# Optimization experiments

Measured on AMD Instinct MI355X. Metric: run time of the kernel, lower is better.

Reference implementation:

```python
import jax, jax.numpy as jnp
import numpy as np

B, S, H, L, V = 128, 512, 1024, 4, 32000


def setup_inputs() -> dict:
    key = jax.random.key(0)
    ks = jax.random.split(key, 7)
    lengths = jax.random.randint(ks[0], (B,), 1, S + 1)
    lengths = lengths.at[0].set(S)  # force max length == S so T is static
    tok = jax.random.randint(ks[1], (B, S), 1, V)  # nonzero tokens inside length
    pos = jnp.arange(S)[None, :]
    x = jnp.where(pos < lengths[:, None], tok, 0)  # 0 = pad (x>0 defines length)
    emb = jax.random.normal(ks[2], (V, H), dtype=jnp.float32) * 0.02
    W_ih = jax.random.normal(ks[3], (L, 4 * H, H), dtype=jnp.float32) / np.float32(np.sqrt(H))
    W_hh = jax.random.normal(ks[4], (L, 4 * H, H), dtype=jnp.float32) / np.float32(np.sqrt(H))
    b_ih = jax.random.normal(ks[5], (L, 4 * H), dtype=jnp.float32) * 0.01
    b_hh = jax.random.normal(ks[6], (L, 4 * H), dtype=jnp.float32) * 0.01
    return {"x": x, "emb": emb, "W_ih": W_ih, "W_hh": W_hh, "b_ih": b_ih, "b_hh": b_hh}


def reference(x, emb, W_ih, W_hh, b_ih, b_hh):
    # lengths and pack's descending sort (pack_padded_sequence, enforce_sorted=False)
    lengths = jnp.sum(x > 0, axis=1)                         # [B]
    sorted_idx = jnp.argsort(-lengths, stable=True)          # sorted (desc) order
    unsort_idx = jnp.argsort(sorted_idx)                     # packed.unsorted_indices

    # Source bug: `start` is never advanced, so every iteration runs a ONE-step
    # stacked LSTM (zero init state) on packed.data[0:bs_t] == t=0 embeddings of
    # the bs_t longest sequences. Compute that single step once on all rows.
    xt = emb[x[sorted_idx, 0]]                               # [B, H] sorted order
    h0 = jnp.zeros_like(xt)                                  # zero initial hidden
    hs, cs = [], []
    for l in range(W_ih.shape[0]):
        gates = xt @ W_ih[l].T + b_ih[l] + h0 @ W_hh[l].T + b_hh[l]
        i, f, g, o = jnp.split(gates, 4, axis=-1)            # torch LSTMCell order
        c = jax.nn.sigmoid(i) * jnp.tanh(g)                  # f * c0 = 0
        h = jax.nn.sigmoid(o) * jnp.tanh(c)
        xt = h
        hs.append(h)
        cs.append(c)

    # output[t, b] = top-layer h for original seq b, zeroed where t >= lengths[b]
    T = x.shape[1]                                           # max length == S
    h_top = xt[unsort_idx]                                   # back to original order
    tmask = (jnp.arange(T)[:, None] < lengths[None, :]).astype(h_top.dtype)  # [T,B]
    output = tmask[:, :, None] * h_top[None, :, :]           # [T, B, H]

    # state from the LAST loop iteration: sorted order, rows >= bs_last zero-padded
    bs_last = jnp.sum(lengths >= T)                          # batch size at t = T-1
    smask = (jnp.arange(x.shape[0]) < bs_last).astype(h_top.dtype)[None, :, None]
    state_h = jnp.stack(hs, axis=0) * smask                  # [L, B, H]
    state_c = jnp.stack(cs, axis=0) * smask                  # [L, B, H]
    return output, state_h, state_c
```

## Files before the change

### kernel.cpp

```cpp
#include <hip/hip_runtime.h>

#define Bn 128
#define Sn 512
#define Hn 1024
#define Ln 4

typedef float nfloat4 __attribute__((ext_vector_type(4)));
typedef __attribute__((ext_vector_type(8))) short short8;
typedef __attribute__((ext_vector_type(4))) float f32x4;

__device__ __forceinline__ float sigmoidf_(float x) { return 1.0f / (1.0f + __expf(-x)); }

__device__ __forceinline__ unsigned short bf16hi(float f) {
  unsigned u = __float_as_uint(f);
  u = u + 0x7FFFu + ((u >> 16) & 1u);
  return (unsigned short)(u >> 16);
}
__device__ __forceinline__ float bf16tof(unsigned short h) {
  return __uint_as_float(((unsigned)h) << 16);
}

__global__ __launch_bounds__(128) void len_kernel(const int* __restrict__ x, int* __restrict__ lengths) {
  const int b = blockIdx.x, t = threadIdx.x;
  int4 v = ((const int4*)x)[b * 128 + t];
  int c = (v.x > 0) + (v.y > 0) + (v.z > 0) + (v.w > 0);
  for (int off = 32; off > 0; off >>= 1) c += __shfl_down(c, off);
  __shared__ int tmp[2];
  if ((t & 63) == 0) tmp[t >> 6] = c;
  __syncthreads();
  if (t == 0) lengths[b] = tmp[0] + tmp[1];
}

__global__ __launch_bounds__(128) void sort_kernel(const int* __restrict__ x, const int* __restrict__ lengths,
                                                   int* __restrict__ rank, int* __restrict__ tok_sorted,
                                                   int* __restrict__ bs_last) {
  __shared__ int sl[128];
  __shared__ int cnt;
  const int b = threadIdx.x;
  const int len = lengths[b];
  sl[b] = len;
  if (b == 0) cnt = 0;
  __syncthreads();
  int r = 0;
  for (int b2 = 0; b2 < 128; b2++) {
    int l2 = sl[b2];
    r += (l2 > len) || (l2 == len && b2 < b);
  }
  rank[b] = r;
  tok_sorted[r] = x[b * Sn];
  if (len >= Sn) atomicAdd(&cnt, 1);
  __syncthreads();
  if (b == 0) bs_last[0] = cnt;
}

__global__ __launch_bounds__(256) void gather_cvt(const int* __restrict__ tok_sorted,
                                                  const float* __restrict__ emb,
                                                  unsigned short* __restrict__ xhi,
                                                  unsigned short* __restrict__ xlo) {
  const int r = blockIdx.x, t = threadIdx.x;
  const int tok = tok_sorted[r];
  float4 v = ((const float4*)emb)[(size_t)tok * 256 + t];
  float f[4] = {v.x, v.y, v.z, v.w};
  unsigned short hh[4], ll[4];
#pragma unroll
  for (int j = 0; j < 4; j++) {
    hh[j] = bf16hi(f[j]);
    ll[j] = bf16hi(f[j] - bf16tof(hh[j]));
  }
  ((ushort4*)xhi)[r * 256 + t] = make_ushort4(hh[0], hh[1], hh[2], hh[3]);
  ((ushort4*)xlo)[r * 256 + t] = make_ushort4(ll[0], ll[1], ll[2], ll[3]);
}

__global__ __launch_bounds__(256) void gemm_mfma(const unsigned short* __restrict__ xhi,
                                                 const unsigned short* __restrict__ xlo,
                                                 const float* __restrict__ Wl,
                                                 float* __restrict__ part) {
  __shared__ unsigned short Whi[64][264];
  __shared__ unsigned short Wlo[64][264];
  const int t = threadIdx.x;
  const int bid = blockIdx.x;
  const int nt = bid % 48;
  const int kc = bid / 48;
  const int q = nt >> 4;
  const int qoff = (q == 0) ? 0 : ((q == 1) ? 2048 : 3072);
  const int mrow0 = qoff + (nt & 15) * 64;
  const int k0 = kc * 256;

#pragma unroll
  for (int i = 0; i < 16; i++) {
    const int vi = i * 256 + t;
    const int c = vi >> 6;
    const int ks4 = (vi & 63) * 4;
    float4 w4 = *(const float4*)&Wl[(size_t)(mrow0 + c) * 1024 + k0 + ks4];
    float f[4] = {w4.x, w4.y, w4.z, w4.w};
    unsigned short hh[4], ll[4];
#pragma unroll
    for (int j = 0; j < 4; j++) {
      hh[j] = bf16hi(f[j]);
      ll[j] = bf16hi(f[j] - bf16tof(hh[j]));
    }
    *(ushort4*)&Whi[c][ks4] = make_ushort4(hh[0], hh[1], hh[2], hh[3]);
    *(ushort4*)&Wlo[c][ks4] = make_ushort4(ll[0], ll[1], ll[2], ll[3]);
  }
  __syncthreads();

  const int w = t >> 6;
  const int l = t & 63;
  const int lrow = l & 15;
  const int lk8 = (l >> 4) * 8;

  f32x4 acc[2][4];
#pragma unroll
  for (int rt = 0; rt < 2; rt++)
#pragma unroll
    for (int ct = 0; ct < 4; ct++) acc[rt][ct] = (f32x4)0.0f;

  const unsigned short* xh0 = xhi + (size_t)(w * 32 + lrow) * 1024 + k0 + lk8;
  const unsigned short* xl0 = xlo + (size_t)(w * 32 + lrow) * 1024 + k0 + lk8;

#pragma unroll
  for (int ks = 0; ks < 8; ks++) {
    const int kk = ks * 32;
    short8 ah[2], al[2], bh[4], bl[4];
#pragma unroll
    for (int rt = 0; rt < 2; rt++) {
      ah[rt] = *(const short8*)(xh0 + rt * 16 * 1024 + kk);
      al[rt] = *(const short8*)(xl0 + rt * 16 * 1024 + kk);
    }
#pragma unroll
    for (int ct = 0; ct < 4; ct++) {
      bh[ct] = *(const short8*)&Whi[ct * 16 + lrow][kk + lk8];
      bl[ct] = *(const short8*)&Wlo[ct * 16 + lrow][kk + lk8];
    }
#pragma unroll
    for (int rt = 0; rt < 2; rt++)
#pragma unroll
      for (int ct = 0; ct < 4; ct++) {
        acc[rt][ct] = __builtin_amdgcn_mfma_f32_16x16x32_bf16(ah[rt], bh[ct], acc[rt][ct], 0, 0, 0);
        acc[rt][ct] = __builtin_amdgcn_mfma_f32_16x16x32_bf16(ah[rt], bl[ct], acc[rt][ct], 0, 0, 0);
        acc[rt][ct] = __builtin_amdgcn_mfma_f32_16x16x32_bf16(al[rt], bh[ct], acc[rt][ct], 0, 0, 0);
      }
  }

  const int rbase = w * 32 + (l >> 4) * 4;
#pragma unroll
  for (int rt = 0; rt < 2; rt++)
#pragma unroll
    for (int ct = 0; ct < 4; ct++) {
      const int m = (nt & 15) * 64 + ct * 16 + lrow;
      *(f32x4*)&part[(((size_t)kc * 3 + q) * 1024 + m) * 128 + rbase + rt * 16] = acc[rt][ct];
    }
}

__global__ __launch_bounds__(256) void act_kernel(const float* __restrict__ part,
                                                  const float* __restrict__ bih,
                                                  const float* __restrict__ bhh,
                                                  const int* __restrict__ bs_last,
                                                  float* __restrict__ xt_out,
                                                  float* __restrict__ sh,
                                                  float* __restrict__ sc,
                                                  unsigned short* __restrict__ xhi_out,
                                                  unsigned short* __restrict__ xlo_out) {
  __shared__ float red[128][12];
  const int t = threadIdx.x;
  const int r = t & 127;
  const int half = t >> 7;
  const int m0 = blockIdx.x * 4;
  float s[3][4];
#pragma unroll
  for (int qq = 0; qq < 3; qq++)
#pragma unroll
    for (int mm = 0; mm < 4; mm++) s[qq][mm] = 0.0f;
#pragma unroll
  for (int k2 = 0; k2 < 2; k2++) {
    const int kcc = half * 2 + k2;
#pragma unroll
    for (int qq = 0; qq < 3; qq++)
#pragma unroll
      for (int mm = 0; mm < 4; mm++)
        s[qq][mm] += part[(((size_t)kcc * 3 + qq) * 1024 + (m0 + mm)) * 128 + r];
  }
  if (half == 1) {
#pragma unroll
    for (int qq = 0; qq < 3; qq++)
#pragma unroll
      for (int mm = 0; mm < 4; mm++) red[r][qq * 4 + mm] = s[qq][mm];
  }
  __syncthreads();
  if (half == 0) {
    const int bs = bs_last[0];
    float hv[4], cv[4];
    unsigned short hh[4], ll[4];
#pragma unroll
    for (int mm = 0; mm < 4; mm++) {
      const int m = m0 + mm;
      const float si = s[0][mm] + red[r][0 * 4 + mm] + bih[m] + bhh[m];
      const float sg = s[1][mm] + red[r][1 * 4 + mm] + bih[2048 + m] + bhh[2048 + m];
      const float so = s[2][mm] + red[r][2 * 4 + mm] + bih[3072 + m] + bhh[3072 + m];
      const float c = sigmoidf_(si) * tanhf(sg);
      const float h = sigmoidf_(so) * tanhf(c);
      hv[mm] = h;
      cv[mm] = c;
      hh[mm] = bf16hi(h);
      ll[mm] = bf16hi(h - bf16tof(hh[mm]));
    }
    const float msk = (r < bs) ? 1.0f : 0.0f;
    *(float4*)&xt_out[(size_t)r * 1024 + m0] = make_float4(hv[0], hv[1], hv[2], hv[3]);
    *(float4*)&sh[(size_t)r * 1024 + m0] =
        make_float4(msk * hv[0], msk * hv[1], msk * hv[2], msk * hv[3]);
    *(float4*)&sc[(size_t)r * 1024 + m0] =
        make_float4(msk * cv[0], msk * cv[1], msk * cv[2], msk * cv[3]);
    *(ushort4*)&xhi_out[(size_t)r * 1024 + m0] = make_ushort4(hh[0], hh[1], hh[2], hh[3]);
    *(ushort4*)&xlo_out[(size_t)r * 1024 + m0] = make_ushort4(ll[0], ll[1], ll[2], ll[3]);
  }
}

__global__ __launch_bounds__(256) void bcast_kernel(const float* __restrict__ hfin,
                                                    const int* __restrict__ lengths,
                                                    const int* __restrict__ rank,
                                                    float* __restrict__ out) {
  const int b = blockIdx.x & 127;
  const int c = blockIdx.x >> 7;
  const int len = lengths[b];
  const int t0 = c * 64;
  nfloat4 v = (nfloat4)0.0f;
  if (t0 < len) v = ((const nfloat4*)hfin)[rank[b] * 256 + threadIdx.x];
  int valid = len - t0;
  valid = valid < 0 ? 0 : (valid > 64 ? 64 : valid);
  nfloat4* p = (nfloat4*)out + ((size_t)t0 * 128 + b) * 256 + threadIdx.x;
  for (int i = 0; i < valid; i++) {
    __builtin_nontemporal_store(v, p);
    p += 32768;
  }
  const nfloat4 z = (nfloat4)0.0f;
  for (int i = valid; i < 64; i++) {
    __builtin_nontemporal_store(z, p);
    p += 32768;
  }
}

extern "C" void kernel_launch(void* const* d_in, const int* in_sizes, int n_in,
                              void* d_out, int out_size, void* d_ws, size_t ws_size,
                              hipStream_t stream) {
  const int* x = (const int*)d_in[0];
  const float* emb = (const float*)d_in[1];
  const float* W_ih = (const float*)d_in[2];
  const float* b_ih = (const float*)d_in[4];
  const float* b_hh = (const float*)d_in[5];

  float* out = (float*)d_out;
  float* sh = out + (size_t)Sn * Bn * Hn;
  float* sc = sh + (size_t)Ln * Bn * Hn;
  float* part = out;
  unsigned short* bfbase = (unsigned short*)(out + (size_t)2097152);
  unsigned short* xhiA = bfbase;
  unsigned short* xloA = bfbase + 131072;
  unsigned short* xhiB = bfbase + 262144;
  unsigned short* xloB = bfbase + 393216;

  char* ws = (char*)d_ws;
  int* lengths = (int*)ws;
  int* rank = lengths + 128;
  int* tok_sorted = rank + 128;
  int* bs_last = tok_sorted + 128;
  float* xtA = (float*)(ws + 4096);
  float* xtB = xtA + 128 * 1024;

  len_kernel<<<128, 128, 0, stream>>>(x, lengths);
  sort_kernel<<<1, 128, 0, stream>>>(x, lengths, rank, tok_sorted, bs_last);
  gather_cvt<<<128, 256, 0, stream>>>(tok_sorted, emb, xhiA, xloA);

  float* xtF[2] = {xtA, xtB};
  unsigned short* hiP[2] = {xhiA, xhiB};
  unsigned short* loP[2] = {xloA, xloB};
  int cur = 0;
  for (int l = 0; l < Ln; l++) {
    const int nxt = cur ^ 1;
    gemm_mfma<<<192, 256, 0, stream>>>(hiP[cur], loP[cur], W_ih + (size_t)l * 4 * Hn * Hn, part);
    act_kernel<<<256, 256, 0, stream>>>(part, b_ih + l * 4 * Hn, b_hh + l * 4 * Hn, bs_last,
                                        xtF[l & 1], sh + (size_t)l * Bn * Hn,
                                        sc + (size_t)l * Bn * Hn, hiP[nxt], loP[nxt]);
    cur = nxt;
  }
  bcast_kernel<<<1024, 256, 0, stream>>>(xtF[1], lengths, rank, out);
}
```

Baseline: 475.9 us.

## Fuse LSTM gate GEMM with activation and overlap padding zero-stores in idle blocks

```diff
diff --git a/kernel.cpp b/kernel.cpp
--- a/kernel.cpp
+++ b/kernel.cpp
@@ -20,37 +20,46 @@
   return __uint_as_float(((unsigned)h) << 16);
 }
 
-__global__ __launch_bounds__(128) void len_kernel(const int* __restrict__ x, int* __restrict__ lengths) {
-  const int b = blockIdx.x, t = threadIdx.x;
-  int4 v = ((const int4*)x)[b * 128 + t];
-  int c = (v.x > 0) + (v.y > 0) + (v.z > 0) + (v.w > 0);
-  for (int off = 32; off > 0; off >>= 1) c += __shfl_down(c, off);
-  __shared__ int tmp[2];
-  if ((t & 63) == 0) tmp[t >> 6] = c;
-  __syncthreads();
-  if (t == 0) lengths[b] = tmp[0] + tmp[1];
-}
-
-__global__ __launch_bounds__(128) void sort_kernel(const int* __restrict__ x, const int* __restrict__ lengths,
-                                                   int* __restrict__ rank, int* __restrict__ tok_sorted,
-                                                   int* __restrict__ bs_last) {
+__global__ __launch_bounds__(1024) void lensort_kernel(const int* __restrict__ x,
+                                                       int* __restrict__ lengths,
+                                                       int* __restrict__ rank,
+                                                       int* __restrict__ tok_sorted,
+                                                       int* __restrict__ bs_last) {
+  __shared__ int pc[128][8];
   __shared__ int sl[128];
   __shared__ int cnt;
-  const int b = threadIdx.x;
-  const int len = lengths[b];
-  sl[b] = len;
-  if (b == 0) cnt = 0;
+  const int t = threadIdx.x;
+  const int row = t >> 3, seg = t & 7;
+  int c = 0;
+  const int4* xp = (const int4*)x + row * 128 + seg * 16;
+#pragma unroll
+  for (int i = 0; i < 16; i++) {
+    int4 v = xp[i];
+    c += (v.x > 0) + (v.y > 0) + (v.z > 0) + (v.w > 0);
+  }
+  pc[row][seg] = c;
+  if (t == 0) cnt = 0;
   __syncthreads();
-  int r = 0;
-  for (int b2 = 0; b2 < 128; b2++) {
-    int l2 = sl[b2];
-    r += (l2 > len) || (l2 == len && b2 < b);
-  }
-  rank[b] = r;
-  tok_sorted[r] = x[b * Sn];
-  if (len >= Sn) atomicAdd(&cnt, 1);
+  int len = 0;
+  if (t < 128) {
+#pragma unroll
+    for (int i = 0; i < 8; i++) len += pc[t][i];
+    sl[t] = len;
+    lengths[t] = len;
+  }
   __syncthreads();
-  if (b == 0) bs_last[0] = cnt;
+  if (t < 128) {
+    int r = 0;
+    for (int b2 = 0; b2 < 128; b2++) {
+      int l2 = sl[b2];
+      r += (l2 > len) || (l2 == len && b2 < t);
+    }
+    rank[t] = r;
+    tok_sorted[r] = x[t * Sn];
+    if (len >= Sn) atomicAdd(&cnt, 1);
+  }
+  __syncthreads();
+  if (t == 0) bs_last[0] = cnt;
 }
 
 __global__ __launch_bounds__(256) void gather_cvt(const int* __restrict__ tok_sorted,
@@ -71,147 +80,145 @@
   ((ushort4*)xlo)[r * 256 + t] = make_ushort4(ll[0], ll[1], ll[2], ll[3]);
 }
 
-__global__ __launch_bounds__(256) void gemm_mfma(const unsigned short* __restrict__ xhi,
-                                                 const unsigned short* __restrict__ xlo,
-                                                 const float* __restrict__ Wl,
-                                                 float* __restrict__ part) {
-  __shared__ unsigned short Whi[64][264];
-  __shared__ unsigned short Wlo[64][264];
-  const int t = threadIdx.x;
-  const int bid = blockIdx.x;
-  const int nt = bid % 48;
-  const int kc = bid / 48;
-  const int q = nt >> 4;
-  const int qoff = (q == 0) ? 0 : ((q == 1) ? 2048 : 3072);
-  const int mrow0 = qoff + (nt & 15) * 64;
-  const int k0 = kc * 256;
-
-#pragma unroll
-  for (int i = 0; i < 16; i++) {
-    const int vi = i * 256 + t;
-    const int c = vi >> 6;
-    const int ks4 = (vi & 63) * 4;
-    float4 w4 = *(const float4*)&Wl[(size_t)(mrow0 + c) * 1024 + k0 + ks4];
-    float f[4] = {w4.x, w4.y, w4.z, w4.w};
-    unsigned short hh[4], ll[4];
-#pragma unroll
-    for (int j = 0; j < 4; j++) {
-      hh[j] = bf16hi(f[j]);
-      ll[j] = bf16hi(f[j] - bf16tof(hh[j]));
-    }
-    *(ushort4*)&Whi[c][ks4] = make_ushort4(hh[0], hh[1], hh[2], hh[3]);
-    *(ushort4*)&Wlo[c][ks4] = make_ushort4(ll[0], ll[1], ll[2], ll[3]);
-  }
-  __syncthreads();
-
-  const int w = t >> 6;
-  const int l = t & 63;
-  const int lrow = l & 15;
-  const int lk8 = (l >> 4) * 8;
-
-  f32x4 acc[2][4];
-#pragma unroll
-  for (int rt = 0; rt < 2; rt++)
-#pragma unroll
-    for (int ct = 0; ct < 4; ct++) acc[rt][ct] = (f32x4)0.0f;
-
-  const unsigned short* xh0 = xhi + (size_t)(w * 32 + lrow) * 1024 + k0 + lk8;
-  const unsigned short* xl0 = xlo + (size_t)(w * 32 + lrow) * 1024 + k0 + lk8;
-
-#pragma unroll
-  for (int ks = 0; ks < 8; ks++) {
-    const int kk = ks * 32;
-    short8 ah[2], al[2], bh[4], bl[4];
-#pragma unroll
-    for (int rt = 0; rt < 2; rt++) {
-      ah[rt] = *(const short8*)(xh0 + rt * 16 * 1024 + kk);
-      al[rt] = *(const short8*)(xl0 + rt * 16 * 1024 + kk);
-    }
-#pragma unroll
-    for (int ct = 0; ct < 4; ct++) {
-      bh[ct] = *(const short8*)&Whi[ct * 16 + lrow][kk + lk8];
-      bl[ct] = *(const short8*)&Wlo[ct * 16 + lrow][kk + lk8];
-    }
-#pragma unroll
-    for (int rt = 0; rt < 2; rt++)
-#pragma unroll
-      for (int ct = 0; ct < 4; ct++) {
-        acc[rt][ct] = __builtin_amdgcn_mfma_f32_16x16x32_bf16(ah[rt], bh[ct], acc[rt][ct], 0, 0, 0);
-        acc[rt][ct] = __builtin_amdgcn_mfma_f32_16x16x32_bf16(ah[rt], bl[ct], acc[rt][ct], 0, 0, 0);
-        acc[rt][ct] = __builtin_amdgcn_mfma_f32_16x16x32_bf16(al[rt], bh[ct], acc[rt][ct], 0, 0, 0);
-      }
-  }
-
-  const int rbase = w * 32 + (l >> 4) * 4;
-#pragma unroll
-  for (int rt = 0; rt < 2; rt++)
-#pragma unroll
-    for (int ct = 0; ct < 4; ct++) {
-      const int m = (nt & 15) * 64 + ct * 16 + lrow;
-      *(f32x4*)&part[(((size_t)kc * 3 + q) * 1024 + m) * 128 + rbase + rt * 16] = acc[rt][ct];
-    }
-}
-
-__global__ __launch_bounds__(256) void act_kernel(const float* __restrict__ part,
+__global__ __launch_bounds__(256) void gemm_fused(const unsigned short* __restrict__ xhi,
+                                                  const unsigned short* __restrict__ xlo,
+                                                  const float* __restrict__ Wl,
                                                   const float* __restrict__ bih,
                                                   const float* __restrict__ bhh,
                                                   const int* __restrict__ bs_last,
+                                                  const int* __restrict__ lengths,
                                                   float* __restrict__ xt_out,
                                                   float* __restrict__ sh,
                                                   float* __restrict__ sc,
                                                   unsigned short* __restrict__ xhi_out,
-                                                  unsigned short* __restrict__ xlo_out) {
-  __shared__ float red[128][12];
+                                                  unsigned short* __restrict__ xlo_out,
+                                                  float* __restrict__ out,
+                                                  const int layer) {
+  __shared__ unsigned short Whi[48][264];
+  __shared__ unsigned short Wlo[48][264];
   const int t = threadIdx.x;
-  const int r = t & 127;
-  const int half = t >> 7;
-  const int m0 = blockIdx.x * 4;
-  float s[3][4];
-#pragma unroll
-  for (int qq = 0; qq < 3; qq++)
-#pragma unroll
-    for (int mm = 0; mm < 4; mm++) s[qq][mm] = 0.0f;
-#pragma unroll
-  for (int k2 = 0; k2 < 2; k2++) {
-    const int kcc = half * 2 + k2;
-#pragma unroll
-    for (int qq = 0; qq < 3; qq++)
-#pragma unroll
-      for (int mm = 0; mm < 4; mm++)
-        s[qq][mm] += part[(((size_t)kcc * 3 + qq) * 1024 + (m0 + mm)) * 128 + r];
-  }
-  if (half == 1) {
-#pragma unroll
-    for (int qq = 0; qq < 3; qq++)
-#pragma unroll
-      for (int mm = 0; mm < 4; mm++) red[r][qq * 4 + mm] = s[qq][mm];
-  }
-  __syncthreads();
-  if (half == 0) {
-    const int bs = bs_last[0];
-    float hv[4], cv[4];
-    unsigned short hh[4], ll[4];
-#pragma unroll
-    for (int mm = 0; mm < 4; mm++) {
-      const int m = m0 + mm;
-      const float si = s[0][mm] + red[r][0 * 4 + mm] + bih[m] + bhh[m];
-      const float sg = s[1][mm] + red[r][1 * 4 + mm] + bih[2048 + m] + bhh[2048 + m];
-      const float so = s[2][mm] + red[r][2 * 4 + mm] + bih[3072 + m] + bhh[3072 + m];
-      const float c = sigmoidf_(si) * tanhf(sg);
-      const float h = sigmoidf_(so) * tanhf(c);
-      hv[mm] = h;
-      cv[mm] = c;
-      hh[mm] = bf16hi(h);
-      ll[mm] = bf16hi(h - bf16tof(hh[mm]));
-    }
-    const float msk = (r < bs) ? 1.0f : 0.0f;
-    *(float4*)&xt_out[(size_t)r * 1024 + m0] = make_float4(hv[0], hv[1], hv[2], hv[3]);
-    *(float4*)&sh[(size_t)r * 1024 + m0] =
-        make_float4(msk * hv[0], msk * hv[1], msk * hv[2], msk * hv[3]);
-    *(float4*)&sc[(size_t)r * 1024 + m0] =
-        make_float4(msk * cv[0], msk * cv[1], msk * cv[2], msk * cv[3]);
-    *(ushort4*)&xhi_out[(size_t)r * 1024 + m0] = make_ushort4(hh[0], hh[1], hh[2], hh[3]);
-    *(ushort4*)&xlo_out[(size_t)r * 1024 + m0] = make_ushort4(ll[0], ll[1], ll[2], ll[3]);
+
+  if (blockIdx.x >= 64) {
+    const int z = blockIdx.x - 64;
+    const int p0 = z * 80;
+    const int tb0 = 32 + layer * 120;
+    const nfloat4 zz = (nfloat4)0.0f;
+    for (int i = 0; i < 80; i++) {
+      const int p = p0 + i;
+      const int tt = tb0 + (p >> 7);
+      const int b = p & 127;
+      if (tt >= lengths[b]) {
+        __builtin_nontemporal_store(zz, (nfloat4*)out + ((size_t)tt * 128 + b) * 256 + t);
+      }
+    }
+    return;
+  }
+
+  const int m0 = blockIdx.x * 16;
+  const int w = t >> 6, l = t & 63;
+  const int lrow = l & 15;
+  const int lk8 = (l >> 4) * 8;
+
+  float4 wreg[12];
+#pragma unroll
+  for (int i = 0; i < 12; i++) {
+    const int vi = i * 256 + t;
+    const int c = vi >> 6;
+    const int k4 = (vi & 63) * 4;
+    const int g = c >> 4;
+    const int wr = ((g == 0) ? 0 : ((g == 1) ? 2048 : 3072)) + m0 + (c & 15);
+    wreg[i] = *(const float4*)&Wl[(size_t)wr * 1024 + k4];
+  }
+
+  f32x4 acc[2][3];
+#pragma unroll
+  for (int rt = 0; rt < 2; rt++)
+#pragma unroll
+    for (int q = 0; q < 3; q++) acc[rt][q] = (f32x4)0.0f;
+
+#pragma unroll
+  for (int kc = 0; kc < 4; kc++) {
+    const int k0 = kc * 256;
+    __syncthreads();
+#pragma unroll
+    for (int i = 0; i < 12; i++) {
+      const int vi = i * 256 + t;
+      const int c = vi >> 6;
+      const int k4 = (vi & 63) * 4;
+      float f[4] = {wreg[i].x, wreg[i].y, wreg[i].z, wreg[i].w};
+      unsigned short hh[4], ll[4];
+#pragma unroll
+      for (int j = 0; j < 4; j++) {
+        hh[j] = bf16hi(f[j]);
+        ll[j] = bf16hi(f[j] - bf16tof(hh[j]));
+      }
+      *(ushort4*)&Whi[c][k4] = make_ushort4(hh[0], hh[1], hh[2], hh[3]);
+      *(ushort4*)&Wlo[c][k4] = make_ushort4(ll[0], ll[1], ll[2], ll[3]);
+    }
+    if (kc < 3) {
+      const int kn = k0 + 256;
+#pragma unroll
+      for (int i = 0; i < 12; i++) {
+        const int vi = i * 256 + t;
+        const int c = vi >> 6;
+        const int k4 = (vi & 63) * 4;
+        const int g = c >> 4;
+        const int wr = ((g == 0) ? 0 : ((g == 1) ? 2048 : 3072)) + m0 + (c & 15);
+        wreg[i] = *(const float4*)&Wl[(size_t)wr * 1024 + kn + k4];
+      }
+    }
+    __syncthreads();
+    const unsigned short* xh0 = xhi + (size_t)(w * 32 + lrow) * 1024 + k0 + lk8;
+    const unsigned short* xl0 = xlo + (size_t)(w * 32 + lrow) * 1024 + k0 + lk8;
+#pragma unroll
+    for (int ks = 0; ks < 8; ks++) {
+      const int kk = ks * 32;
+      short8 ah[2], al[2], bh[3], bl[3];
+#pragma unroll
+      for (int rt = 0; rt < 2; rt++) {
+        ah[rt] = *(const short8*)(xh0 + rt * 16 * 1024 + kk);
+        al[rt] = *(const short8*)(xl0 + rt * 16 * 1024 + kk);
+      }
+#pragma unroll
+      for (int q = 0; q < 3; q++) {
+        bh[q] = *(const short8*)&Whi[q * 16 + lrow][kk + lk8];
+        bl[q] = *(const short8*)&Wlo[q * 16 + lrow][kk + lk8];
+      }
+#pragma unroll
+      for (int rt = 0; rt < 2; rt++)
+#pragma unroll
+        for (int q = 0; q < 3; q++) {
+          acc[rt][q] = __builtin_amdgcn_mfma_f32_16x16x32_bf16(ah[rt], bh[q], acc[rt][q], 0, 0, 0);
+          acc[rt][q] = __builtin_amdgcn_mfma_f32_16x16x32_bf16(ah[rt], bl[q], acc[rt][q], 0, 0, 0);
+          acc[rt][q] = __builtin_amdgcn_mfma_f32_16x16x32_bf16(al[rt], bh[q], acc[rt][q], 0, 0, 0);
+        }
+    }
+  }
+
+  const int bs = bs_last[0];
+  const int m = m0 + lrow;
+  const float bi = bih[m] + bhh[m];
+  const float bg = bih[2048 + m] + bhh[2048 + m];
+  const float bo = bih[3072 + m] + bhh[3072 + m];
+#pragma unroll
+  for (int rt = 0; rt < 2; rt++) {
+    const int rb = w * 32 + rt * 16 + (l >> 4) * 4;
+#pragma unroll
+    for (int j = 0; j < 4; j++) {
+      const int r = rb + j;
+      const float iv = acc[rt][0][j] + bi;
+      const float gv = acc[rt][1][j] + bg;
+      const float ov = acc[rt][2][j] + bo;
+      const float cc = sigmoidf_(iv) * tanhf(gv);
+      const float hh = sigmoidf_(ov) * tanhf(cc);
+      const float msk = (r < bs) ? 1.0f : 0.0f;
+      xt_out[(size_t)r * 1024 + m] = hh;
+      sh[(size_t)r * 1024 + m] = msk * hh;
+      sc[(size_t)r * 1024 + m] = msk * cc;
+      const unsigned short hb = bf16hi(hh);
+      xhi_out[(size_t)r * 1024 + m] = hb;
+      xlo_out[(size_t)r * 1024 + m] = bf16hi(hh - bf16tof(hb));
+    }
   }
 }
 
@@ -223,19 +230,22 @@
   const int c = blockIdx.x >> 7;
   const int len = lengths[b];
   const int t0 = c * 64;
-  nfloat4 v = (nfloat4)0.0f;
-  if (t0 < len) v = ((const nfloat4*)hfin)[rank[b] * 256 + threadIdx.x];
-  int valid = len - t0;
-  valid = valid < 0 ? 0 : (valid > 64 ? 64 : valid);
-  nfloat4* p = (nfloat4*)out + ((size_t)t0 * 128 + b) * 256 + threadIdx.x;
-  for (int i = 0; i < valid; i++) {
-    __builtin_nontemporal_store(v, p);
-    p += 32768;
-  }
-  const nfloat4 z = (nfloat4)0.0f;
-  for (int i = valid; i < 64; i++) {
-    __builtin_nontemporal_store(z, p);
-    p += 32768;
+  if (t0 < len) {
+    const nfloat4 v = ((const nfloat4*)hfin)[rank[b] * 256 + threadIdx.x];
+    const int hi = (len < t0 + 64) ? len : (t0 + 64);
+    nfloat4* p = (nfloat4*)out + ((size_t)t0 * 128 + b) * 256 + threadIdx.x;
+    for (int tt = t0; tt < hi; tt++) {
+      __builtin_nontemporal_store(v, p);
+      p += 32768;
+    }
+  }
+  if (c == 0 && len < 32) {
+    const nfloat4 z = (nfloat4)0.0f;
+    nfloat4* pz = (nfloat4*)out + ((size_t)len * 128 + b) * 256 + threadIdx.x;
+    for (int tt = len; tt < 32; tt++) {
+      __builtin_nontemporal_store(z, pz);
+      pz += 32768;
+    }
   }
 }
 
@@ -251,7 +261,6 @@
   float* out = (float*)d_out;
   float* sh = out + (size_t)Sn * Bn * Hn;
   float* sc = sh + (size_t)Ln * Bn * Hn;
-  float* part = out;
   unsigned short* bfbase = (unsigned short*)(out + (size_t)2097152);
   unsigned short* xhiA = bfbase;
   unsigned short* xloA = bfbase + 131072;
@@ -266,8 +275,7 @@
   float* xtA = (float*)(ws + 4096);
   float* xtB = xtA + 128 * 1024;
 
-  len_kernel<<<128, 128, 0, stream>>>(x, lengths);
-  sort_kernel<<<1, 128, 0, stream>>>(x, lengths, rank, tok_sorted, bs_last);
+  lensort_kernel<<<1, 1024, 0, stream>>>(x, lengths, rank, tok_sorted, bs_last);
   gather_cvt<<<128, 256, 0, stream>>>(tok_sorted, emb, xhiA, xloA);
 
   float* xtF[2] = {xtA, xtB};
@@ -276,10 +284,10 @@
   int cur = 0;
   for (int l = 0; l < Ln; l++) {
     const int nxt = cur ^ 1;
-    gemm_mfma<<<192, 256, 0, stream>>>(hiP[cur], loP[cur], W_ih + (size_t)l * 4 * Hn * Hn, part);
-    act_kernel<<<256, 256, 0, stream>>>(part, b_ih + l * 4 * Hn, b_hh + l * 4 * Hn, bs_last,
+    gemm_fused<<<256, 256, 0, stream>>>(hiP[cur], loP[cur], W_ih + (size_t)l * 4 * Hn * Hn,
+                                        b_ih + l * 4 * Hn, b_hh + l * 4 * Hn, bs_last, lengths,
                                         xtF[l & 1], sh + (size_t)l * Bn * Hn,
-                                        sc + (size_t)l * Bn * Hn, hiP[nxt], loP[nxt]);
+                                        sc + (size_t)l * Bn * Hn, hiP[nxt], loP[nxt], out, l);
     cur = nxt;
   }
   bcast_kernel<<<1024, 256, 0, stream>>>(xtF[1], lengths, rank, out);
```

New measurement: 513.4 us. 7.9% more time.
